# Kernel optimization log

Measured on AMD Instinct MI355X. Metric: run time of the kernel, lower is better.

Reference implementation:

```python
import jax, jax.numpy as jnp
import numpy as np

N, F_IN = 50000, 128      # nodes, input channels
H, C = 4, 32              # attention heads, out channels per head (concat -> H*C = 128)
E = 800000                # directed edges (before self loops)
NEG_SLOPE = 0.2
EPS = 1e-5                # GraphNorm eps


def setup_inputs() -> dict:
    key = jax.random.key(0)
    ks = jax.random.split(key, 9)
    s = 1.0 / np.sqrt(F_IN)
    return {
        "x": jax.random.normal(ks[0], (N, F_IN), jnp.float32),
        "edge_index": jax.random.randint(ks[1], (2, E), 0, N, jnp.int32),
        "W_l": jax.random.uniform(ks[2], (F_IN, H * C), jnp.float32, -s, s),  # source proj
        "W_r": jax.random.uniform(ks[3], (F_IN, H * C), jnp.float32, -s, s),  # target proj
        "att": jax.random.uniform(ks[4], (H, C), jnp.float32, -s, s),         # GATv2 attention vector a
        "bias": jnp.zeros((H * C,), jnp.float32),
        "gn_weight": jnp.ones((H * C,), jnp.float32),
        "gn_bias": jnp.zeros((H * C,), jnp.float32),
        "gn_mean_scale": jnp.ones((H * C,), jnp.float32),
    }


def _gatv2_graphnorm(x, edge_index, W_l, W_r, att, bias, gn_weight, gn_bias, gn_mean_scale):
    n = x.shape[0]
    # add self loops (add_self_loops=True)
    ar = jnp.arange(n, dtype=edge_index.dtype)
    src = jnp.concatenate([edge_index[0], ar])  # message source j
    dst = jnp.concatenate([edge_index[1], ar])  # message target i

    x_l = (x @ W_l).reshape(n, H, C)  # source-side features
    x_r = (x @ W_r).reshape(n, H, C)  # target-side features

    # GATv2 score: a . LeakyReLU(W_l x_j + W_r x_i), per edge per head  [E+N, H]
    e = jax.nn.leaky_relu(x_l[src] + x_r[dst], NEG_SLOPE)
    score = jnp.einsum("ehc,hc->eh", e, att)

    # softmax over each destination's incoming edges (segment softmax)
    smax = jax.ops.segment_max(score, dst, num_segments=n)
    ex = jnp.exp(score - smax[dst])
    denom = jax.ops.segment_sum(ex, dst, num_segments=n)
    alpha = ex / denom[dst]  # [E+N, H]

    # aggregate messages: out_i = sum_j alpha_ij * (W_l x_j)
    out = jax.ops.segment_sum(alpha[:, :, None] * x_l[src], dst, num_segments=n)
    out = out.reshape(n, H * C) + bias  # concat heads

    # GraphNorm (single graph): per-feature mean/var over all nodes
    mean = out.mean(axis=0)
    centered = out - gn_mean_scale * mean
    var = (centered * centered).mean(axis=0)
    return gn_weight * centered * jax.lax.rsqrt(var + EPS) + gn_bias


def reference(x, edge_index, W_l, W_r, att, bias, gn_weight, gn_bias, gn_mean_scale):
    return _gatv2_graphnorm(x, edge_index, W_l, W_r, att, bias, gn_weight, gn_bias, gn_mean_scale)
```

## Files before the change

kernel.cpp:

```cpp
#include <hip/hip_runtime.h>
#include <hip/hip_bf16.h>
#include <math.h>

#define N_NODES 50000
#define F_IN 128
#define HC 128
#define N_EDGES 800000
#define E_TOT (N_EDGES + N_NODES)
#define E_HALF (E_TOT / 2)
#define NEG_SLOPE 0.2f
#define GN_EPS 1e-5f
#define DEG_STRIDE 16
#define CAP 64
#define GB ((N_NODES + 127) / 128)
#define EB2 ((E_HALF + 511) / 512)
#define FUSED_GRID (GB + EB2)

typedef __attribute__((ext_vector_type(8))) short short8;
typedef __attribute__((ext_vector_type(4))) float floatx4;

__device__ inline ushort f2bf(float f) {
    unsigned u = __float_as_uint(f);
    u += 0x7FFF + ((u >> 16) & 1);
    return (ushort)(u >> 16);
}

__global__ __launch_bounds__(256) void wprep_k(const float* __restrict__ Wl,
                                               const float* __restrict__ Wr,
                                               ushort* __restrict__ wtl,
                                               ushort* __restrict__ wtr) {
    int gid = blockIdx.x * 256 + threadIdx.x;
    int k = gid >> 7, n = gid & 127;
    wtl[n * 128 + k] = f2bf(Wl[gid]);
    wtr[n * 128 + k] = f2bf(Wr[gid]);
}

__global__ __launch_bounds__(512) void eg_k(const int* __restrict__ ei,
                                            int* __restrict__ deg16,
                                            ushort* __restrict__ csrp,
                                            const float* __restrict__ x,
                                            const ushort* __restrict__ wtl,
                                            const ushort* __restrict__ wtr,
                                            ushort* __restrict__ xlb,
                                            ushort* __restrict__ xrb) {
    __shared__ ushort Wt[2][128][136];
    const int bi = blockIdx.x;
    const int tid = threadIdx.x;
    const bool isG = (bi < 3 * GB) && (bi % 3 == 1);

    if (!isG) {
        const int eb = bi - ((bi < 3 * GB) ? (bi + 1) / 3 : GB);
        int gid = eb * 512 + tid;
        if (gid >= E_HALF) return;
        {
            int src = ei[gid], dst = ei[N_EDGES + gid];
            int r = atomicAdd(&deg16[dst * DEG_STRIDE], 1);
            if (r < CAP) csrp[dst * CAP + r] = (ushort)src;
        }
        {
            int e = gid + E_HALF;
            int src, dst;
            if (e < N_EDGES) { src = ei[e]; dst = ei[N_EDGES + e]; }
            else             { src = dst = e - N_EDGES; }
            int r = atomicAdd(&deg16[dst * DEG_STRIDE], 1);
            if (r < CAP) csrp[dst * CAP + r] = (ushort)src;
        }
        return;
    }

    const int gb = bi / 3;
#pragma unroll
    for (int i = 0; i < 4; ++i) {
        int idx = i * 512 + tid;
        int n = idx >> 4, k8 = (idx & 15) * 8;
        *(int4*)&Wt[0][n][k8] = *(const int4*)(wtl + n * 128 + k8);
        *(int4*)&Wt[1][n][k8] = *(const int4*)(wtr + n * 128 + k8);
    }
    __syncthreads();

    const int w = tid >> 6, lane = tid & 63;
    const int quad = lane >> 4, l16 = lane & 15;
    const int rbase = gb * 128 + w * 16;
    const int grow = rbase + l16;
    const float* ap = x + (size_t)(grow < N_NODES ? grow : (N_NODES - 1)) * F_IN + quad * 8;

    floatx4 accL[8], accR[8];
#pragma unroll
    for (int nt = 0; nt < 8; ++nt) {
        accL[nt] = (floatx4){0.f, 0.f, 0.f, 0.f};
        accR[nt] = (floatx4){0.f, 0.f, 0.f, 0.f};
    }

#pragma unroll
    for (int ks = 0; ks < 4; ++ks) {
        float4 a0 = *(const float4*)(ap + ks * 32 + 0);
        float4 a1 = *(const float4*)(ap + ks * 32 + 4);
        short8 af;
        af[0] = (short)f2bf(a0.x); af[1] = (short)f2bf(a0.y);
        af[2] = (short)f2bf(a0.z); af[3] = (short)f2bf(a0.w);
        af[4] = (short)f2bf(a1.x); af[5] = (short)f2bf(a1.y);
        af[6] = (short)f2bf(a1.z); af[7] = (short)f2bf(a1.w);
#pragma unroll
        for (int nt = 0; nt < 8; ++nt) {
            short8 bfl = *(const short8*)&Wt[0][nt * 16 + l16][ks * 32 + quad * 8];
            short8 bfr = *(const short8*)&Wt[1][nt * 16 + l16][ks * 32 + quad * 8];
            accL[nt] = __builtin_amdgcn_mfma_f32_16x16x32_bf16(af, bfl, accL[nt], 0, 0, 0);
            accR[nt] = __builtin_amdgcn_mfma_f32_16x16x32_bf16(af, bfr, accR[nt], 0, 0, 0);
        }
    }
#pragma unroll
    for (int r = 0; r < 4; ++r) {
        int gro = rbase + quad * 4 + r;
        if (gro < N_NODES) {
            ushort* opl = xlb + (size_t)gro * HC + l16;
            ushort* opr = xrb + (size_t)gro * HC + l16;
#pragma unroll
            for (int nt = 0; nt < 8; ++nt) {
                opl[nt * 16] = f2bf(accL[nt][r]);
                opr[nt * 16] = f2bf(accR[nt][r]);
            }
        }
    }
}

__global__ __launch_bounds__(256) void attn_k(const ushort* __restrict__ xlb,
                                              const ushort* __restrict__ xrb,
                                              const int* __restrict__ deg16,
                                              const ushort* __restrict__ csrp,
                                              const float* __restrict__ att,
                                              const float* __restrict__ bias,
                                              float* __restrict__ out) {
    const int wid = threadIdx.x >> 6, lane = threadIdx.x & 63;
    const int dst = blockIdx.x * 4 + wid;
    if (dst >= N_NODES) return;
    const int e = lane >> 4, s = lane & 15;
    float xrv[8], av[8];
    {
        int4 xv = *(const int4*)(xrb + (size_t)dst * HC + s * 8);
        xrv[0] = __uint_as_float(((unsigned)xv.x) << 16);
        xrv[1] = __uint_as_float(((unsigned)xv.x) & 0xffff0000u);
        xrv[2] = __uint_as_float(((unsigned)xv.y) << 16);
        xrv[3] = __uint_as_float(((unsigned)xv.y) & 0xffff0000u);
        xrv[4] = __uint_as_float(((unsigned)xv.z) << 16);
        xrv[5] = __uint_as_float(((unsigned)xv.z) & 0xffff0000u);
        xrv[6] = __uint_as_float(((unsigned)xv.w) << 16);
        xrv[7] = __uint_as_float(((unsigned)xv.w) & 0xffff0000u);
        float4 a0 = *(const float4*)(att + s * 8);
        float4 a1 = *(const float4*)(att + s * 8 + 4);
        av[0] = a0.x; av[1] = a0.y; av[2] = a0.z; av[3] = a0.w;
        av[4] = a1.x; av[5] = a1.y; av[6] = a1.z; av[7] = a1.w;
    }
    float l = 0.f;
    float acc[8] = {0.f, 0.f, 0.f, 0.f, 0.f, 0.f, 0.f, 0.f};
    const int nk = min(deg16[dst * DEG_STRIDE], CAP);
    const int sv = (int)csrp[dst * CAP + lane];

#define EDGE_STEP(rv, valid)                                                   \
    {                                                                          \
        float f0 = __uint_as_float(((unsigned)(rv).x) << 16);                  \
        float f1 = __uint_as_float(((unsigned)(rv).x) & 0xffff0000u);          \
        float f2 = __uint_as_float(((unsigned)(rv).y) << 16);                  \
        float f3 = __uint_as_float(((unsigned)(rv).y) & 0xffff0000u);          \
        float f4 = __uint_as_float(((unsigned)(rv).z) << 16);                  \
        float f5 = __uint_as_float(((unsigned)(rv).z) & 0xffff0000u);          \
        float f6 = __uint_as_float(((unsigned)(rv).w) << 16);                  \
        float f7 = __uint_as_float(((unsigned)(rv).w) & 0xffff0000u);          \
        float t, part;                                                         \
        t = f0 + xrv[0]; t = t > 0.f ? t : NEG_SLOPE * t; part = av[0] * t;    \
        t = f1 + xrv[1]; t = t > 0.f ? t : NEG_SLOPE * t; part += av[1] * t;   \
        t = f2 + xrv[2]; t = t > 0.f ? t : NEG_SLOPE * t; part += av[2] * t;   \
        t = f3 + xrv[3]; t = t > 0.f ? t : NEG_SLOPE * t; part += av[3] * t;   \
        t = f4 + xrv[4]; t = t > 0.f ? t : NEG_SLOPE * t; part += av[4] * t;   \
        t = f5 + xrv[5]; t = t > 0.f ? t : NEG_SLOPE * t; part += av[5] * t;   \
        t = f6 + xrv[6]; t = t > 0.f ? t : NEG_SLOPE * t; part += av[6] * t;   \
        t = f7 + xrv[7]; t = t > 0.f ? t : NEG_SLOPE * t; part += av[7] * t;   \
        part += __shfl_xor(part, 1, 4);                                        \
        part += __shfl_xor(part, 2, 4);                                        \
        float p = (valid) ? __expf(part) : 0.f;                                \
        l += p;                                                                \
        acc[0] += p * f0; acc[1] += p * f1; acc[2] += p * f2; acc[3] += p * f3;\
        acc[4] += p * f4; acc[5] += p * f5; acc[6] += p * f6; acc[7] += p * f7;\
    }

    int j = 0;
    for (; j + 8 <= nk; j += 8) {
        int s0 = __shfl(sv, j + e, 64);
        int s1 = __shfl(sv, j + 4 + e, 64);
        int4 r0 = *(const int4*)(xlb + (size_t)s0 * HC + s * 8);
        int4 r1 = *(const int4*)(xlb + (size_t)s1 * HC + s * 8);
        EDGE_STEP(r0, true);
        EDGE_STEP(r1, true);
    }
    for (; j < nk; j += 4) {
        int idx = j + e;
        bool valid = idx < nk;
        int s0 = __shfl(sv, valid ? idx : 0, 64);
        int4 r0 = *(const int4*)(xlb + (size_t)s0 * HC + s * 8);
        EDGE_STEP(r0, valid);
    }
#undef EDGE_STEP

    l += __shfl_xor(l, 16, 64);
    l += __shfl_xor(l, 32, 64);
#pragma unroll
    for (int c = 0; c < 8; ++c) {
        acc[c] += __shfl_xor(acc[c], 16, 64);
        acc[c] += __shfl_xor(acc[c], 32, 64);
    }
    if (e == 0) {
        float inv = 1.0f / l;
        float4 b0 = *(const float4*)(bias + s * 8);
        float4 b1 = *(const float4*)(bias + s * 8 + 4);
        float4 o0 = make_float4(acc[0] * inv + b0.x, acc[1] * inv + b0.y,
                                acc[2] * inv + b0.z, acc[3] * inv + b0.w);
        float4 o1 = make_float4(acc[4] * inv + b1.x, acc[5] * inv + b1.y,
                                acc[6] * inv + b1.z, acc[7] * inv + b1.w);
        *(float4*)(out + (size_t)dst * HC + s * 8)     = o0;
        *(float4*)(out + (size_t)dst * HC + s * 8 + 4) = o1;
    }
}

__global__ __launch_bounds__(256) void stats_k(const float* __restrict__ out,
                                               float* __restrict__ gsum,
                                               float* __restrict__ gsumsq) {
    int f = threadIdx.x & 127;
    int half = threadIdx.x >> 7;
    float s = 0.f, s2 = 0.f;
    for (int r = blockIdx.x * 2 + half; r < N_NODES; r += gridDim.x * 2) {
        float v = out[(size_t)r * HC + f];
        s += v; s2 += v * v;
    }
    __shared__ float l1[256], l2[256];
    l1[threadIdx.x] = s; l2[threadIdx.x] = s2;
    __syncthreads();
    if (threadIdx.x < 128) {
        s  = l1[threadIdx.x] + l1[threadIdx.x + 128];
        s2 = l2[threadIdx.x] + l2[threadIdx.x + 128];
        atomicAdd(&gsum[f], s);
        atomicAdd(&gsumsq[f], s2);
    }
}

__global__ __launch_bounds__(256) void norm_k(float* __restrict__ out,
                                              const float* __restrict__ gsum,
                                              const float* __restrict__ gsumsq,
                                              const float* __restrict__ gw,
                                              const float* __restrict__ gb,
                                              const float* __restrict__ gms) {
    int f = threadIdx.x & 127;
    int half = threadIdx.x >> 7;
    const float invN = 1.0f / (float)N_NODES;
    float mean = gsum[f] * invN;
    float msq  = gsumsq[f] * invN;
    float g = gms[f];
    float var = msq - 2.f * g * mean * mean + g * g * mean * mean;
    float rstd = rsqrtf(var + GN_EPS);
    float a = gw[f] * rstd;
    float b = gb[f] - a * g * mean;
    for (int r = blockIdx.x * 2 + half; r < N_NODES; r += gridDim.x * 2) {
        size_t o = (size_t)r * HC + f;
        out[o] = a * out[o] + b;
    }
}

extern "C" void kernel_launch(void* const* d_in, const int* in_sizes, int n_in,
                              void* d_out, int out_size, void* d_ws, size_t ws_size,
                              hipStream_t stream) {
    const float* x    = (const float*)d_in[0];
    const int*   ei   = (const int*)d_in[1];
    const float* Wl   = (const float*)d_in[2];
    const float* Wr   = (const float*)d_in[3];
    const float* att  = (const float*)d_in[4];
    const float* bias = (const float*)d_in[5];
    const float* gw   = (const float*)d_in[6];
    const float* gb   = (const float*)d_in[7];
    const float* gms  = (const float*)d_in[8];
    float* out = (float*)d_out;

    ushort* xlb   = (ushort*)d_ws;
    ushort* xrb   = xlb + (size_t)N_NODES * HC;
    float*  gsum   = (float*)(xrb + (size_t)N_NODES * HC);
    float*  gsumsq = gsum + HC;
    int*    deg16  = (int*)(gsumsq + HC);
    size_t  zero_bytes = (size_t)(HC + HC) * 4 + (size_t)N_NODES * DEG_STRIDE * 4;
    ushort* csrp = (ushort*)(deg16 + (size_t)N_NODES * DEG_STRIDE);
    ushort* wtl  = csrp + (size_t)N_NODES * CAP;
    ushort* wtr  = wtl + 16384;

    hipMemsetAsync((void*)gsum, 0, zero_bytes, stream);
    hipLaunchKernelGGL(wprep_k, dim3(64), dim3(256), 0, stream,
                       Wl, Wr, wtl, wtr);
    hipLaunchKernelGGL(eg_k, dim3(FUSED_GRID), dim3(512), 0, stream,
                       ei, deg16, csrp, x, wtl, wtr, xlb, xrb);
    hipLaunchKernelGGL(attn_k, dim3(N_NODES / 4), dim3(256), 0, stream,
                       xlb, xrb, deg16, csrp, att, bias, out);
    hipLaunchKernelGGL(stats_k, dim3(256), dim3(256), 0, stream,
                       out, gsum, gsumsq);
    hipLaunchKernelGGL(norm_k, dim3(512), dim3(256), 0, stream,
                       out, gsum, gsumsq, gw, gb, gms);
}
```

Baseline: 215.8 us.

## Fuse GraphNorm stats and normalize via grid barrier; fold memset and self-loops into init

Merges the stats and normalize kernels into one kernel that keeps each thread's column values in registers, synchronizes all 512 blocks with a global atomic barrier, then writes normalized output without re-reading it from memory. The memset is replaced by an init kernel that also seeds self-loops directly (degree 1, slot 0 = self), so the edge-grouping pass only handles real edges. This removes a kernel launch, a memset, and one full read of the output, but depends on all 512 blocks being co-resident for the spin barrier to avoid deadlock and adds register pressure.

```diff
diff --git a/kernel.cpp b/kernel.cpp
--- a/kernel.cpp
+++ b/kernel.cpp
@@ -6,15 +6,17 @@
 #define F_IN 128
 #define HC 128
 #define N_EDGES 800000
-#define E_TOT (N_EDGES + N_NODES)
-#define E_HALF (E_TOT / 2)
+#define E_HALF_R (N_EDGES / 2)
 #define NEG_SLOPE 0.2f
 #define GN_EPS 1e-5f
 #define DEG_STRIDE 16
 #define CAP 64
 #define GB ((N_NODES + 127) / 128)
-#define EB2 ((E_HALF + 511) / 512)
-#define FUSED_GRID (GB + EB2)
+#define EBR ((E_HALF_R + 511) / 512)
+#define FUSED_GRID (GB + EBR)
+#define SN_BLOCKS 512
+#define SN_SLOTS (SN_BLOCKS * 2)
+#define SN_K 49
 
 typedef __attribute__((ext_vector_type(8))) short short8;
 typedef __attribute__((ext_vector_type(4))) float floatx4;
@@ -25,14 +27,26 @@
     return (ushort)(u >> 16);
 }
 
-__global__ __launch_bounds__(256) void wprep_k(const float* __restrict__ Wl,
-                                               const float* __restrict__ Wr,
-                                               ushort* __restrict__ wtl,
-                                               ushort* __restrict__ wtr) {
+__global__ __launch_bounds__(256) void init_k(const float* __restrict__ Wl,
+                                              const float* __restrict__ Wr,
+                                              ushort* __restrict__ wtl,
+                                              ushort* __restrict__ wtr,
+                                              int* __restrict__ deg16,
+                                              ushort* __restrict__ csrp,
+                                              float* __restrict__ gsum,
+                                              unsigned* __restrict__ bar) {
     int gid = blockIdx.x * 256 + threadIdx.x;
-    int k = gid >> 7, n = gid & 127;
-    wtl[n * 128 + k] = f2bf(Wl[gid]);
-    wtr[n * 128 + k] = f2bf(Wr[gid]);
+    if (gid < 16384) {
+        int k = gid >> 7, n = gid & 127;
+        wtl[n * 128 + k] = f2bf(Wl[gid]);
+        wtr[n * 128 + k] = f2bf(Wr[gid]);
+    }
+    if (gid < 256) gsum[gid] = 0.f;
+    if (gid == 0) *bar = 0u;
+    if (gid < N_NODES) {
+        deg16[gid * DEG_STRIDE] = 1;
+        csrp[(size_t)gid * CAP] = (ushort)gid;
+    }
 }
 
 __global__ __launch_bounds__(512) void eg_k(const int* __restrict__ ei,
@@ -46,24 +60,22 @@
     __shared__ ushort Wt[2][128][136];
     const int bi = blockIdx.x;
     const int tid = threadIdx.x;
-    const bool isG = (bi < 3 * GB) && (bi % 3 == 1);
+    const bool isG = (bi % 3 == 1);
 
     if (!isG) {
-        const int eb = bi - ((bi < 3 * GB) ? (bi + 1) / 3 : GB);
+        const int eb = bi - (bi + 1) / 3;
         int gid = eb * 512 + tid;
-        if (gid >= E_HALF) return;
+        if (gid >= E_HALF_R) return;
         {
             int src = ei[gid], dst = ei[N_EDGES + gid];
             int r = atomicAdd(&deg16[dst * DEG_STRIDE], 1);
-            if (r < CAP) csrp[dst * CAP + r] = (ushort)src;
+            if (r < CAP) csrp[(size_t)dst * CAP + r] = (ushort)src;
         }
         {
-            int e = gid + E_HALF;
-            int src, dst;
-            if (e < N_EDGES) { src = ei[e]; dst = ei[N_EDGES + e]; }
-            else             { src = dst = e - N_EDGES; }
+            int e = gid + E_HALF_R;
+            int src = ei[e], dst = ei[N_EDGES + e];
             int r = atomicAdd(&deg16[dst * DEG_STRIDE], 1);
-            if (r < CAP) csrp[dst * CAP + r] = (ushort)src;
+            if (r < CAP) csrp[(size_t)dst * CAP + r] = (ushort)src;
         }
         return;
     }
@@ -153,7 +165,7 @@
     float l = 0.f;
     float acc[8] = {0.f, 0.f, 0.f, 0.f, 0.f, 0.f, 0.f, 0.f};
     const int nk = min(deg16[dst * DEG_STRIDE], CAP);
-    const int sv = (int)csrp[dst * CAP + lane];
+    const int sv = (int)csrp[(size_t)dst * CAP + lane];
 
 #define EDGE_STEP(rv, valid)                                                   \
     {                                                                          \
@@ -220,46 +232,52 @@
     }
 }
 
-__global__ __launch_bounds__(256) void stats_k(const float* __restrict__ out,
-                                               float* __restrict__ gsum,
-                                               float* __restrict__ gsumsq) {
-    int f = threadIdx.x & 127;
-    int half = threadIdx.x >> 7;
+__global__ __launch_bounds__(256) void sn_k(float* __restrict__ out,
+                                            float* __restrict__ gsum,
+                                            float* __restrict__ gsumsq,
+                                            const float* __restrict__ gw,
+                                            const float* __restrict__ gb,
+                                            const float* __restrict__ gms,
+                                            unsigned* __restrict__ bar) {
+    const int f = threadIdx.x & 127;
+    const int half = threadIdx.x >> 7;
+    const int slot = blockIdx.x * 2 + half;
+    float v[SN_K];
     float s = 0.f, s2 = 0.f;
-    for (int r = blockIdx.x * 2 + half; r < N_NODES; r += gridDim.x * 2) {
-        float v = out[(size_t)r * HC + f];
-        s += v; s2 += v * v;
+#pragma unroll
+    for (int k = 0; k < SN_K; ++k) {
+        int r = slot + k * SN_SLOTS;
+        float t = (r < N_NODES) ? out[(size_t)r * HC + f] : 0.f;
+        v[k] = t;
+        s += t; s2 += t * t;
     }
     __shared__ float l1[256], l2[256];
     l1[threadIdx.x] = s; l2[threadIdx.x] = s2;
     __syncthreads();
     if (threadIdx.x < 128) {
-        s  = l1[threadIdx.x] + l1[threadIdx.x + 128];
-        s2 = l2[threadIdx.x] + l2[threadIdx.x + 128];
-        atomicAdd(&gsum[f], s);
-        atomicAdd(&gsumsq[f], s2);
-    }
-}
-
-__global__ __launch_bounds__(256) void norm_k(float* __restrict__ out,
-                                              const float* __restrict__ gsum,
-                                              const float* __restrict__ gsumsq,
-                                              const float* __restrict__ gw,
-                                              const float* __restrict__ gb,
-                                              const float* __restrict__ gms) {
-    int f = threadIdx.x & 127;
-    int half = threadIdx.x >> 7;
+        atomicAdd(&gsum[f],   l1[threadIdx.x] + l1[threadIdx.x + 128]);
+        atomicAdd(&gsumsq[f], l2[threadIdx.x] + l2[threadIdx.x + 128]);
+    }
+    __threadfence();
+    __syncthreads();
+    if (threadIdx.x == 0) {
+        __hip_atomic_fetch_add(bar, 1u, __ATOMIC_ACQ_REL, __HIP_MEMORY_SCOPE_AGENT);
+        while (__hip_atomic_load(bar, __ATOMIC_ACQUIRE, __HIP_MEMORY_SCOPE_AGENT) < SN_BLOCKS) {}
+    }
+    __syncthreads();
+
     const float invN = 1.0f / (float)N_NODES;
-    float mean = gsum[f] * invN;
-    float msq  = gsumsq[f] * invN;
+    float mean = __hip_atomic_load(&gsum[f],   __ATOMIC_RELAXED, __HIP_MEMORY_SCOPE_AGENT) * invN;
+    float msq  = __hip_atomic_load(&gsumsq[f], __ATOMIC_RELAXED, __HIP_MEMORY_SCOPE_AGENT) * invN;
     float g = gms[f];
     float var = msq - 2.f * g * mean * mean + g * g * mean * mean;
     float rstd = rsqrtf(var + GN_EPS);
     float a = gw[f] * rstd;
     float b = gb[f] - a * g * mean;
-    for (int r = blockIdx.x * 2 + half; r < N_NODES; r += gridDim.x * 2) {
-        size_t o = (size_t)r * HC + f;
-        out[o] = a * out[o] + b;
+#pragma unroll
+    for (int k = 0; k < SN_K; ++k) {
+        int r = slot + k * SN_SLOTS;
+        if (r < N_NODES) out[(size_t)r * HC + f] = a * v[k] + b;
     }
 }
 
@@ -282,20 +300,17 @@
     float*  gsum   = (float*)(xrb + (size_t)N_NODES * HC);
     float*  gsumsq = gsum + HC;
     int*    deg16  = (int*)(gsumsq + HC);
-    size_t  zero_bytes = (size_t)(HC + HC) * 4 + (size_t)N_NODES * DEG_STRIDE * 4;
     ushort* csrp = (ushort*)(deg16 + (size_t)N_NODES * DEG_STRIDE);
     ushort* wtl  = csrp + (size_t)N_NODES * CAP;
     ushort* wtr  = wtl + 16384;
-
-    hipMemsetAsync((void*)gsum, 0, zero_bytes, stream);
-    hipLaunchKernelGGL(wprep_k, dim3(64), dim3(256), 0, stream,
-                       Wl, Wr, wtl, wtr);
+    unsigned* bar = (unsigned*)(wtr + 16384);
+
+    hipLaunchKernelGGL(init_k, dim3(196), dim3(256), 0, stream,
+                       Wl, Wr, wtl, wtr, deg16, csrp, gsum, bar);
     hipLaunchKernelGGL(eg_k, dim3(FUSED_GRID), dim3(512), 0, stream,
                        ei, deg16, csrp, x, wtl, wtr, xlb, xrb);
     hipLaunchKernelGGL(attn_k, dim3(N_NODES / 4), dim3(256), 0, stream,
                        xlb, xrb, deg16, csrp, att, bias, out);
-    hipLaunchKernelGGL(stats_k, dim3(256), dim3(256), 0, stream,
-                       out, gsum, gsumsq);
-    hipLaunchKernelGGL(norm_k, dim3(512), dim3(256), 0, stream,
-                       out, gsum, gsumsq, gw, gb, gms);
-}
+    hipLaunchKernelGGL(sn_k, dim3(SN_BLOCKS), dim3(256), 0, stream,
+                       out, gsum, gsumsq, gw, gb, gms, bar);
+}
```

New measurement: 238.8 us. +10.7%, slower.
